# Performance work log

Measured on AMD Instinct MI355X. Metric: run time of the kernel, lower is better.

## Reference

```python
import jax, jax.numpy as jnp
import numpy as np


def setup_inputs() -> dict:
    key = jax.random.key(0)
    ks = jax.random.split(key, 7)
    S, N, D_in, D_out = 8, 5000, 128, 128
    theta = jax.random.uniform(ks[0], (S,), dtype=jnp.float32)
    T_slices = jax.random.normal(ks[1], (S, N, N), dtype=jnp.float32)
    x = jax.random.normal(ks[2], (N, D_in), dtype=jnp.float32)
    a = (jax.random.uniform(ks[3], (N, N), dtype=jnp.float32) < 0.05).astype(jnp.float32)
    # PReLU per-feature slope (torch default init is 0.25; random here)
    alpha = jax.random.uniform(ks[4], (D_in,), dtype=jnp.float32) * 0.5
    W = jax.random.normal(ks[5], (D_out, D_in), dtype=jnp.float32) * (1.0 / np.sqrt(D_in))
    b = jax.random.normal(ks[6], (D_out,), dtype=jnp.float32) * 0.01
    return {"theta": theta, "T_slices": T_slices, "x": x, "a": a,
            "alpha": alpha, "W": W, "b": b}


def reference(theta, T_slices, x, a, alpha, W, b):
    # weighted sum of diffusion slices: q[i,j] = sum_s theta[s] * T[s,i,j]
    q = jnp.einsum('s,sij->ij', theta, T_slices)
    q = q * a  # elementwise mask (sparsification pattern)
    out = q @ x  # dense matmul == sparse.mm on masked matrix (same math)
    # PReLU with per-feature (last-dim) slopes
    out = jnp.where(out >= 0, out, alpha * out)
    # Linear: out @ W.T + b
    return out @ W.T + b
```

## Files before the change

kernel.cpp:

```cpp
#include <hip/hip_runtime.h>

#define SS 8
#define NN 5000
#define NNSQ 25000000
#define DD 128
#define RB 8
#define JS 4
#define JT 128
#define TPB 10
#define RG 625

typedef float f4 __attribute__((ext_vector_type(4)));

typedef const __attribute__((address_space(1))) void glb_void;
typedef __attribute__((address_space(3))) void lds_void;

__device__ __forceinline__ void gld_lds16(const void* g, void* l) {
    __builtin_amdgcn_global_load_lds((glb_void*)g, (lds_void*)l, 16, 0, 0);
}

#define VMCNT9  asm volatile("s_waitcnt vmcnt(9)" ::: "memory")
#define VMCNT0  asm volatile("s_waitcnt vmcnt(0)" ::: "memory")
#define LGKM0   asm volatile("s_waitcnt lgkmcnt(0)" ::: "memory")
#define SB0     __builtin_amdgcn_sched_barrier(0)

__global__ __launch_bounds__(256, 2)
void diffuse_spmm(const float* __restrict__ theta,
                  const float* __restrict__ Tm,
                  const float* __restrict__ x,
                  const float* __restrict__ am,
                  float* __restrict__ ws)
{
    __shared__ float stg[2][SS * RB * 128];
    __shared__ float qv[2][RB * 128];

    const int t    = threadIdx.x;
    const int wid  = t >> 6;
    const int lane = t & 63;
    const int rg   = blockIdx.x % RG;
    const int js   = blockIdx.x / RG;
    const int i0   = rg * RB;
    const int tile0 = js * TPB;

    const int ar = (wid << 1) + (lane >> 5);
    const int aj = (lane & 31) << 2;
    const int h  = t >> 5;
    const int d0 = (t & 31) << 2;

    float th[SS];
#pragma unroll
    for (int s = 0; s < SS; ++s) th[s] = theta[s];

    auto stage_dma = [&](int m) {
        const int j = (tile0 + m) * JT + aj;
        if (j < NN) {
            const size_t goff = (size_t)(i0 + ar) * NN + j;
#pragma unroll
            for (int s = 0; s < SS; ++s)
                gld_lds16(Tm + (size_t)s * NNSQ + goff,
                          &stg[m & 1][s * (RB * 128) + (wid << 1) * 128]);
        }
    };

    auto aload = [&](int m) -> f4 {
        const int j = (tile0 + m) * JT + aj;
        f4 v = (f4)(0.0f);
        if (j < NN) v = *(const f4*)(am + (size_t)(i0 + ar) * NN + j);
        return v;
    };

    auto qcompute = [&](int m, f4 sa) {
        const int j = (tile0 + m) * JT + aj;
        const int lbase = ar * 128 + aj;
        f4 ssum = (*(const f4*)&stg[m & 1][0 * (RB * 128) + lbase]) * th[0];
#pragma unroll
        for (int s = 1; s < SS; ++s)
            ssum += (*(const f4*)&stg[m & 1][s * (RB * 128) + lbase]) * th[s];
        f4 q = sa * ssum;
        if (j >= NN) q = (f4)(0.0f);
        *(f4*)&qv[m & 1][ar * 128 + aj] = q;
    };

    f4 acc[RB];
#pragma unroll
    for (int r = 0; r < RB; ++r) acc[r] = (f4)(0.0f);

    stage_dma(0);
    f4 a0 = aload(0);
    SB0;
    stage_dma(1);
    SB0;
    VMCNT9;
    SB0;
    qcompute(0, a0);
    LGKM0;
    __builtin_amdgcn_s_barrier();

    for (int k = 0; k < TPB; ++k) {
        f4 xv[16];
        {
            const int jb = (tile0 + k) * JT + (h << 4);
#pragma unroll
            for (int q = 0; q < 16; ++q) {
                const int j = jb + q;
                if (j < NN) xv[q] = *(const f4*)(x + (size_t)j * DD + d0);
                else        xv[q] = (f4)(0.0f);
            }
        }
        f4 sa = (f4)(0.0f);
        if (k + 1 < TPB) sa = aload(k + 1);
        SB0;
        if (k + 2 < TPB) stage_dma(k + 2);
        SB0;

        const float* qp = &qv[k & 1][0];
#pragma unroll
        for (int qc = 0; qc < 4; ++qc) {
#pragma unroll
            for (int r = 0; r < RB; ++r) {
                f4 q = *(const f4*)&qp[r * 128 + (h << 4) + (qc << 2)];
                acc[r] += q.x * xv[qc * 4 + 0];
                acc[r] += q.y * xv[qc * 4 + 1];
                acc[r] += q.z * xv[qc * 4 + 2];
                acc[r] += q.w * xv[qc * 4 + 3];
            }
        }

        if (k + 1 < TPB) {
            if (k + 2 < TPB) { VMCNT9; } else { VMCNT0; }
            SB0;
            qcompute(k + 1, sa);
            LGKM0;
            __builtin_amdgcn_s_barrier();
        }
    }

#pragma unroll
    for (int r = 0; r < RB; ++r)
#pragma unroll
        for (int c = 0; c < 4; ++c)
            acc[r][c] += __shfl_xor(acc[r][c], 32);

    float* red = &stg[0][0];
    __syncthreads();
    if (wid > 0 && lane < 32) {
#pragma unroll
        for (int r = 0; r < RB; ++r)
            *(f4*)&red[((wid - 1) * RB + r) * 128 + d0] = acc[r];
    }
    __syncthreads();
    if (wid == 0 && lane < 32) {
#pragma unroll
        for (int r = 0; r < RB; ++r) {
            f4 v = acc[r];
#pragma unroll
            for (int p = 0; p < 3; ++p)
                v += *(const f4*)&red[(p * RB + r) * 128 + d0];
            *(f4*)&ws[(((size_t)js * RG + rg) * RB + r) * DD + d0] = v;
        }
    }
}

__global__ __launch_bounds__(256, 2)
void prelu_linear(const float* __restrict__ alpha,
                  const float* __restrict__ W,
                  const float* __restrict__ b,
                  const float* __restrict__ ws,
                  float* __restrict__ out)
{
    __shared__ float Wt[128 * 129];
    __shared__ float p[16 * 128];
    const int t  = threadIdx.x;
    const int i0 = blockIdx.x * 16;

#pragma unroll
    for (int it = 0; it < 16; ++it) {
        int f  = (it * 256 + t) * 4;
        int d  = f >> 7;
        int kk = f & 127;
        f4 w4 = *(const f4*)(W + f);
        Wt[(kk + 0) * 129 + d] = w4.x;
        Wt[(kk + 1) * 129 + d] = w4.y;
        Wt[(kk + 2) * 129 + d] = w4.z;
        Wt[(kk + 3) * 129 + d] = w4.w;
    }

#pragma unroll
    for (int it = 0; it < 2; ++it) {
        int fi  = it * 256 + t;
        int row = i0 + (fi >> 5);
        int dc  = (fi & 31) << 2;
        if (row < NN) {
            size_t base = (size_t)row * DD + dc;
            f4 v = *(const f4*)(ws + base);
            v += *(const f4*)(ws + base + (size_t)1 * RG * RB * DD);
            v += *(const f4*)(ws + base + (size_t)2 * RG * RB * DD);
            v += *(const f4*)(ws + base + (size_t)3 * RG * RB * DD);
            f4 al = *(const f4*)(alpha + dc);
            f4 pv;
            pv.x = v.x >= 0.f ? v.x : al.x * v.x;
            pv.y = v.y >= 0.f ? v.y : al.y * v.y;
            pv.z = v.z >= 0.f ? v.z : al.z * v.z;
            pv.w = v.w >= 0.f ? v.w : al.w * v.w;
            *(f4*)&p[(row - i0) * 128 + dc] = pv;
        }
    }
    __syncthreads();

    const int d  = t & 127;
    const int rq = t >> 7;
    const float bv = b[d];
    float acc[8];
#pragma unroll
    for (int ri = 0; ri < 8; ++ri) acc[ri] = 0.f;
#pragma unroll 8
    for (int k = 0; k < 128; ++k) {
        float wv = Wt[k * 129 + d];
#pragma unroll
        for (int ri = 0; ri < 8; ++ri)
            acc[ri] += p[(rq * 8 + ri) * 128 + k] * wv;
    }
#pragma unroll
    for (int ri = 0; ri < 8; ++ri) {
        int row = i0 + rq * 8 + ri;
        if (row < NN) out[(size_t)row * DD + d] = acc[ri] + bv;
    }
}

extern "C" void kernel_launch(void* const* d_in, const int* in_sizes, int n_in,
                              void* d_out, int out_size, void* d_ws, size_t ws_size,
                              hipStream_t stream) {
    const float* theta = (const float*)d_in[0];
    const float* T     = (const float*)d_in[1];
    const float* x     = (const float*)d_in[2];
    const float* a     = (const float*)d_in[3];
    const float* alpha = (const float*)d_in[4];
    const float* W     = (const float*)d_in[5];
    const float* b     = (const float*)d_in[6];
    float* out = (float*)d_out;
    float* ws  = (float*)d_ws;

    dim3 blk(256);
    dim3 g1(RG * JS);
    diffuse_spmm<<<g1, blk, 0, stream>>>(theta, T, x, a, ws);

    dim3 g2((NN + 15) / 16);
    prelu_linear<<<g2, blk, 0, stream>>>(alpha, W, b, ws, out);
}
```

Baseline: 276.6 us.

## Give each wave its own column slice of the tile to drop block barriers

Each wave now stages, computes and consumes q for its own 32-column slice of the 128-column tile, so q is produced and read only within one wave. This removes the per-tile s_barrier and lgkmcnt wait, and the double-buffered q array shrinks to one per-wave buffer. The trade-off is that global loads per wave now cover 32-float row segments instead of 128-float contiguous runs, which makes coalescing worse. The wait count changes to vmcnt(8) to match the new order of outstanding loads.

```diff
diff --git a/kernel.cpp b/kernel.cpp
--- a/kernel.cpp
+++ b/kernel.cpp
@@ -19,10 +19,9 @@
     __builtin_amdgcn_global_load_lds((glb_void*)g, (lds_void*)l, 16, 0, 0);
 }
 
-#define VMCNT9  asm volatile("s_waitcnt vmcnt(9)" ::: "memory")
-#define VMCNT0  asm volatile("s_waitcnt vmcnt(0)" ::: "memory")
-#define LGKM0   asm volatile("s_waitcnt lgkmcnt(0)" ::: "memory")
-#define SB0     __builtin_amdgcn_sched_barrier(0)
+#define VMCNT8 asm volatile("s_waitcnt vmcnt(8)" ::: "memory")
+#define VMCNT0 asm volatile("s_waitcnt vmcnt(0)" ::: "memory")
+#define SB0    __builtin_amdgcn_sched_barrier(0)
 
 __global__ __launch_bounds__(256, 2)
 void diffuse_spmm(const float* __restrict__ theta,
@@ -31,8 +30,8 @@
                   const float* __restrict__ am,
                   float* __restrict__ ws)
 {
-    __shared__ float stg[2][SS * RB * 128];
-    __shared__ float qv[2][RB * 128];
+    __shared__ float stg[2][SS][4][RB * 32];
+    __shared__ float qld[4][RB * 32];
 
     const int t    = threadIdx.x;
     const int wid  = t >> 6;
@@ -41,44 +40,44 @@
     const int js   = blockIdx.x / RG;
     const int i0   = rg * RB;
     const int tile0 = js * TPB;
-
-    const int ar = (wid << 1) + (lane >> 5);
-    const int aj = (lane & 31) << 2;
-    const int h  = t >> 5;
-    const int d0 = (t & 31) << 2;
+    const int jw   = wid << 5;
+
+    const int qrow = lane >> 3;
+    const int qcol = (lane & 7) << 2;
+    const int lb   = (qrow << 5) + qcol;
+    const int d0   = (lane & 31) << 2;
+    const int jh   = lane >> 5;
 
     float th[SS];
 #pragma unroll
     for (int s = 0; s < SS; ++s) th[s] = theta[s];
 
     auto stage_dma = [&](int m) {
-        const int j = (tile0 + m) * JT + aj;
-        if (j < NN) {
-            const size_t goff = (size_t)(i0 + ar) * NN + j;
+        const int jg = (tile0 + m) * JT + jw + qcol;
+        if (jg < NN) {
+            const size_t goff = (size_t)(i0 + qrow) * NN + jg;
 #pragma unroll
             for (int s = 0; s < SS; ++s)
-                gld_lds16(Tm + (size_t)s * NNSQ + goff,
-                          &stg[m & 1][s * (RB * 128) + (wid << 1) * 128]);
+                gld_lds16(Tm + (size_t)s * NNSQ + goff, &stg[m & 1][s][wid][0]);
         }
     };
 
     auto aload = [&](int m) -> f4 {
-        const int j = (tile0 + m) * JT + aj;
+        const int jg = (tile0 + m) * JT + jw + qcol;
         f4 v = (f4)(0.0f);
-        if (j < NN) v = *(const f4*)(am + (size_t)(i0 + ar) * NN + j);
+        if (jg < NN) v = *(const f4*)(am + (size_t)(i0 + qrow) * NN + jg);
         return v;
     };
 
     auto qcompute = [&](int m, f4 sa) {
-        const int j = (tile0 + m) * JT + aj;
-        const int lbase = ar * 128 + aj;
-        f4 ssum = (*(const f4*)&stg[m & 1][0 * (RB * 128) + lbase]) * th[0];
+        const int jg = (tile0 + m) * JT + jw + qcol;
+        f4 ssum = (*(const f4*)&stg[m & 1][0][wid][lb]) * th[0];
 #pragma unroll
         for (int s = 1; s < SS; ++s)
-            ssum += (*(const f4*)&stg[m & 1][s * (RB * 128) + lbase]) * th[s];
+            ssum += (*(const f4*)&stg[m & 1][s][wid][lb]) * th[s];
         f4 q = sa * ssum;
-        if (j >= NN) q = (f4)(0.0f);
-        *(f4*)&qv[m & 1][ar * 128 + aj] = q;
+        if (jg >= NN) q = (f4)(0.0f);
+        *(f4*)&qld[wid][lb] = q;
     };
 
     f4 acc[RB];
@@ -86,52 +85,47 @@
     for (int r = 0; r < RB; ++r) acc[r] = (f4)(0.0f);
 
     stage_dma(0);
-    f4 a0 = aload(0);
+    SB0;
+    f4 sa = aload(0);
     SB0;
     stage_dma(1);
     SB0;
-    VMCNT9;
-    SB0;
-    qcompute(0, a0);
-    LGKM0;
-    __builtin_amdgcn_s_barrier();
+    VMCNT8;
+    SB0;
+    qcompute(0, sa);
 
     for (int k = 0; k < TPB; ++k) {
         f4 xv[16];
         {
-            const int jb = (tile0 + k) * JT + (h << 4);
+            const int jbase = (tile0 + k) * JT + jw + (jh << 4);
 #pragma unroll
             for (int q = 0; q < 16; ++q) {
-                const int j = jb + q;
+                const int j = jbase + q;
                 if (j < NN) xv[q] = *(const f4*)(x + (size_t)j * DD + d0);
                 else        xv[q] = (f4)(0.0f);
             }
         }
-        f4 sa = (f4)(0.0f);
         if (k + 1 < TPB) sa = aload(k + 1);
         SB0;
         if (k + 2 < TPB) stage_dma(k + 2);
         SB0;
 
-        const float* qp = &qv[k & 1][0];
 #pragma unroll
         for (int qc = 0; qc < 4; ++qc) {
 #pragma unroll
             for (int r = 0; r < RB; ++r) {
-                f4 q = *(const f4*)&qp[r * 128 + (h << 4) + (qc << 2)];
-                acc[r] += q.x * xv[qc * 4 + 0];
-                acc[r] += q.y * xv[qc * 4 + 1];
-                acc[r] += q.z * xv[qc * 4 + 2];
-                acc[r] += q.w * xv[qc * 4 + 3];
+                f4 q4 = *(const f4*)&qld[wid][(r << 5) + (jh << 4) + (qc << 2)];
+                acc[r] += q4.x * xv[qc * 4 + 0];
+                acc[r] += q4.y * xv[qc * 4 + 1];
+                acc[r] += q4.z * xv[qc * 4 + 2];
+                acc[r] += q4.w * xv[qc * 4 + 3];
             }
         }
 
         if (k + 1 < TPB) {
-            if (k + 2 < TPB) { VMCNT9; } else { VMCNT0; }
+            if (k + 2 < TPB) { VMCNT8; } else { VMCNT0; }
             SB0;
             qcompute(k + 1, sa);
-            LGKM0;
-            __builtin_amdgcn_s_barrier();
         }
     }
 
@@ -141,21 +135,21 @@
         for (int c = 0; c < 4; ++c)
             acc[r][c] += __shfl_xor(acc[r][c], 32);
 
-    float* red = &stg[0][0];
     __syncthreads();
-    if (wid > 0 && lane < 32) {
+    float* red = (float*)&stg[0][0][0][0];
+    if (wid > 0 && jh == 0) {
 #pragma unroll
         for (int r = 0; r < RB; ++r)
-            *(f4*)&red[((wid - 1) * RB + r) * 128 + d0] = acc[r];
+            *(f4*)&red[((wid - 1) * RB + r) * DD + d0] = acc[r];
     }
     __syncthreads();
-    if (wid == 0 && lane < 32) {
+    if (wid == 0 && jh == 0) {
 #pragma unroll
         for (int r = 0; r < RB; ++r) {
             f4 v = acc[r];
 #pragma unroll
             for (int p = 0; p < 3; ++p)
-                v += *(const f4*)&red[(p * RB + r) * 128 + d0];
+                v += *(const f4*)&red[(p * RB + r) * DD + d0];
             *(f4*)&ws[(((size_t)js * RG + rg) * RB + r) * DD + d0] = v;
         }
     }
```

After: 296.4 us. 7.2% more time.
